# Performance work log

Measured on AMD Instinct MI355X. Metric: run time of the kernel, lower is better.

The kernel has to match this reference:

```python
import jax, jax.numpy as jnp
import numpy as np

B, L, D, H = 2, 2048, 1024, 16
HD = D // H  # head dim = 64


def setup_inputs() -> dict:
    key = jax.random.key(0)
    ks = jax.random.split(key, 5)
    s = 1.0 / np.sqrt(D)
    return {
        "x": jax.random.normal(ks[0], (B, L, D), dtype=jnp.float32),
        "mask": jnp.ones((B, 1, 1, L), dtype=jnp.int32),
        "Wq": jax.random.normal(ks[1], (D, D), dtype=jnp.float32) * s,
        "bq": jnp.zeros((D,), dtype=jnp.float32),
        "Wk": jax.random.normal(ks[2], (D, D), dtype=jnp.float32) * s,
        "bk": jnp.zeros((D,), dtype=jnp.float32),
        "Wv": jax.random.normal(ks[3], (D, D), dtype=jnp.float32) * s,
        "bv": jnp.zeros((D,), dtype=jnp.float32),
        "Wo": jax.random.normal(ks[4], (D, D), dtype=jnp.float32) * s,
        "bo": jnp.zeros((D,), dtype=jnp.float32),
    }


def reference(x, mask, Wq, bq, Wk, bk, Wv, bv, Wo, bo):
    Bx, Lx = x.shape[0], x.shape[1]
    # torch nn.Linear: y = x @ W.T + b
    q = (jnp.einsum("bld,ed->ble", x, Wq) + bq).reshape(Bx, Lx, H, HD).transpose(0, 2, 1, 3)
    k = (jnp.einsum("bld,ed->ble", x, Wk) + bk).reshape(Bx, Lx, H, HD).transpose(0, 2, 1, 3)
    v = (jnp.einsum("bld,ed->ble", x, Wv) + bv).reshape(Bx, Lx, H, HD).transpose(0, 2, 1, 3)
    # [B, H, L, L] scores
    scores = jnp.einsum("bhqd,bhkd->bhqk", q, k) / np.sqrt(HD).astype(np.float32)
    # faithful to original: masked positions are set to the tiny value 1e-9 (not -inf)
    scores = jnp.where(mask == 0, jnp.float32(1e-9), scores)
    attn = jax.nn.softmax(scores, axis=-1)
    # dropout_prob=0.0 -> identity (eval mode)
    out = jnp.einsum("bhqk,bhkd->bhqd", attn, v)  # [B, H, L, HD]
    out = out.transpose(0, 2, 1, 3).reshape(Bx, Lx, D)
    return jnp.einsum("bld,ed->ble", out, Wo) + bo
```

## Files before the change

### kernel.cpp

```cpp
#include <hip/hip_runtime.h>
#include <hip/hip_bf16.h>

typedef _Float16 f16;
typedef _Float16 f16x8 __attribute__((ext_vector_type(8)));
typedef _Float16 f16x4 __attribute__((ext_vector_type(4)));
typedef _Float16 f16x2 __attribute__((ext_vector_type(2)));
typedef float f32x4 __attribute__((ext_vector_type(4)));
typedef int i32x4 __attribute__((ext_vector_type(4)));

#define LDS_LOAD16(gptr, lptr)                                                             \
  __builtin_amdgcn_global_load_lds(                                                        \
      (const __attribute__((address_space(1))) unsigned int*)(gptr),                       \
      (__attribute__((address_space(3))) unsigned int*)(lptr), 16, 0, 0)

#define ALPHA 0.18033688f
#define MASKVAL 1.44269504e-9f

__global__ __launch_bounds__(256) void conv_all(const float* __restrict__ x,
                                                const float* __restrict__ Wq,
                                                const float* __restrict__ Wk,
                                                const float* __restrict__ Wv,
                                                const float* __restrict__ Wo,
                                                f16* __restrict__ xh, f16* __restrict__ wqh,
                                                f16* __restrict__ wkh, f16* __restrict__ wvh,
                                                f16* __restrict__ woh) {
  int i = blockIdx.x * 256 + threadIdx.x;
  const float* src;
  f16* dst;
  int off;
  if (i < 524288) {
    src = x; dst = xh; off = i;
  } else {
    int j = i - 524288;
    int w = j >> 17;
    off = j & 131071;
    src = (w == 0) ? Wq : (w == 1) ? Wk : (w == 2) ? Wv : Wo;
    dst = (w == 0) ? wqh : (w == 1) ? wkh : (w == 2) ? wvh : woh;
  }
  const float4* s4 = (const float4*)src;
  float4 a = s4[2 * off];
  float4 b = s4[2 * off + 1];
  f16x8 o = {(f16)a.x, (f16)a.y, (f16)a.z, (f16)a.w,
             (f16)b.x, (f16)b.y, (f16)b.z, (f16)b.w};
  *(f16x8*)(dst + (size_t)off * 8) = o;
}

__global__ __launch_bounds__(256) void gemm_qkv(const f16* __restrict__ A,
                                                const f16* __restrict__ W0,
                                                const f16* __restrict__ W1,
                                                const f16* __restrict__ W2,
                                                const float* __restrict__ b0,
                                                const float* __restrict__ b1,
                                                const float* __restrict__ b2,
                                                f16* __restrict__ qo, f16* __restrict__ ko,
                                                f16* __restrict__ vo) {
  constexpr int K = 1024, BM = 128, BK = 32;
  __shared__ f16 aT[BM * BK];
  __shared__ f16 bT[BM * BK];
  const int z = blockIdx.z;
  const f16* Bw = (z == 0) ? W0 : (z == 1) ? W1 : W2;
  const float* bias = (z == 0) ? b0 : (z == 1) ? b1 : b2;
  const int tid = threadIdx.x, wid = tid >> 6, lane = tid & 63;
  const int mb = blockIdx.y * BM, nb = blockIdx.x * BM;
  const int wr = wid >> 1, wc = wid & 1;
  const int lr = lane & 15, hi = lane >> 4;

  f32x4 acc[4][4] = {};

  const int r0 = tid >> 2, s0 = tid & 3;
  const int ci1 = 256 + tid, r1 = ci1 >> 2, s1 = ci1 & 3;

  for (int kt = 0; kt < K / BK; ++kt) {
    __syncthreads();
    const int kb = kt * BK;
    LDS_LOAD16(A + (size_t)(mb + r0) * K + kb + s0 * 8, (char*)aT + wid * 1024);
    LDS_LOAD16(Bw + (size_t)(nb + r0) * K + kb + s0 * 8, (char*)bT + wid * 1024);
    LDS_LOAD16(A + (size_t)(mb + r1) * K + kb + s1 * 8, (char*)aT + 4096 + wid * 1024);
    LDS_LOAD16(Bw + (size_t)(nb + r1) * K + kb + s1 * 8, (char*)bT + 4096 + wid * 1024);
    __syncthreads();

    f16x8 af[4], bf[4];
#pragma unroll
    for (int i = 0; i < 4; ++i) af[i] = *(const f16x8*)&aT[(wr * 64 + i * 16 + lr) * BK + hi * 8];
#pragma unroll
    for (int j = 0; j < 4; ++j) bf[j] = *(const f16x8*)&bT[(wc * 64 + j * 16 + lr) * BK + hi * 8];
    __builtin_amdgcn_s_setprio(1);
#pragma unroll
    for (int i = 0; i < 4; ++i)
#pragma unroll
      for (int j = 0; j < 4; ++j)
        acc[i][j] = __builtin_amdgcn_mfma_f32_16x16x32_f16(af[i], bf[j], acc[i][j], 0, 0, 0);
    __builtin_amdgcn_s_setprio(0);
  }

  const float scale = (z == 0) ? ALPHA : 1.0f;
#pragma unroll
  for (int i = 0; i < 4; ++i) {
#pragma unroll
    for (int j = 0; j < 4; ++j) {
      const int row = mb + wr * 64 + i * 16 + hi * 4;
      const int col = nb + wc * 64 + j * 16 + lr;
      const float bv = bias[col];
      const int hh = col >> 6, dd = col & 63;
      if (z == 2) {
        const int bb = row >> 11, l = row & 2047;
        f16x4 v4;
#pragma unroll
        for (int r = 0; r < 4; ++r) v4[r] = (f16)(acc[i][j][r] + bv);
        *(f16x4*)(vo + ((((size_t)bb * 16 + hh) * 64 + dd) * 2048 + l)) = v4;
      } else {
        f16* o = z ? ko : qo;
#pragma unroll
        for (int r = 0; r < 4; ++r) {
          const int m2 = row + r;
          const int bb = m2 >> 11, l = m2 & 2047;
          o[((((size_t)bb * 16 + hh) * 2048 + l) * 64) + dd] = (f16)((acc[i][j][r] + bv) * scale);
        }
      }
    }
  }
}

__global__ __launch_bounds__(256) void gemm_o(const f16* __restrict__ A,
                                              const f16* __restrict__ W,
                                              const float* __restrict__ bias,
                                              float* __restrict__ out) {
  constexpr int K = 1024, N = 1024, BK = 32;
  __shared__ f16 aT[64 * BK];
  __shared__ f16 bT[128 * BK];
  const int tid = threadIdx.x, wid = tid >> 6, lane = tid & 63;
  const int lr = lane & 15, hi = lane >> 4;
  const int mb = blockIdx.y * 64, nb = blockIdx.x * 128;
  const int wr = wid >> 1, wc = wid & 1;
  f32x4 acc[2][4] = {};
  const int ra = tid >> 2, sa = tid & 3;
  const int rb1 = (256 + tid) >> 2, sb1 = (256 + tid) & 3;

  for (int kt = 0; kt < K / BK; ++kt) {
    __syncthreads();
    const int kb = kt * BK;
    LDS_LOAD16(A + (size_t)(mb + ra) * K + kb + sa * 8, (char*)aT + wid * 1024);
    LDS_LOAD16(W + (size_t)(nb + ra) * K + kb + sa * 8, (char*)bT + wid * 1024);
    LDS_LOAD16(W + (size_t)(nb + rb1) * K + kb + sb1 * 8, (char*)bT + 4096 + wid * 1024);
    __syncthreads();
    f16x8 af[2], bf[4];
#pragma unroll
    for (int i = 0; i < 2; ++i) af[i] = *(const f16x8*)&aT[(wr * 32 + i * 16 + lr) * BK + hi * 8];
#pragma unroll
    for (int j = 0; j < 4; ++j) bf[j] = *(const f16x8*)&bT[(wc * 64 + j * 16 + lr) * BK + hi * 8];
    __builtin_amdgcn_s_setprio(1);
#pragma unroll
    for (int i = 0; i < 2; ++i)
#pragma unroll
      for (int j = 0; j < 4; ++j)
        acc[i][j] = __builtin_amdgcn_mfma_f32_16x16x32_f16(af[i], bf[j], acc[i][j], 0, 0, 0);
    __builtin_amdgcn_s_setprio(0);
  }
#pragma unroll
  for (int i = 0; i < 2; ++i)
#pragma unroll
    for (int j = 0; j < 4; ++j) {
      const int col = nb + wc * 64 + j * 16 + lr;
      const float bv = bias[col];
#pragma unroll
      for (int r = 0; r < 4; ++r)
        out[(size_t)(mb + wr * 32 + i * 16 + hi * 4 + r) * N + col] = acc[i][j][r] + bv;
    }
}

__global__ __launch_bounds__(128, 2) void attn2w(const f16* __restrict__ Qh,
                                                 const f16* __restrict__ Kh,
                                                 const f16* __restrict__ Vt,
                                                 const int* __restrict__ mask,
                                                 f16* __restrict__ Oa) {
  constexpr int L = 2048, HD = 64, H = 16, NT = L / 64;
  __shared__ __align__(16) char ldsb[32768];

  const int tid = threadIdx.x, w = tid >> 6, lane = tid & 63;
  const int lr = lane & 15, hi = lane >> 4;
  const int sw = lr & 7;
  const bool oddhi = (hi & 1) != 0;

  const int bid = blockIdx.x;
  const int head = (bid & 7) * 4 + (bid >> 8);
  const int qb = (bid >> 3) & 31;
  const int b = head >> 4, h = head & 15;
  const int qr0 = qb * 64 + w * 32;

  const f16* Qb = Qh + (size_t)head * L * HD;
  const f16* Kb = Kh + (size_t)head * L * HD;
  const f16* Vb = Vt + (size_t)head * HD * L;
  const int* mrow = mask + b * L;

  int mred = 1;
  {
    const int4* m4 = (const int4*)mrow;
#pragma unroll
    for (int j = 0; j < 8; ++j) {
      int4 v = m4[lane + j * 64];
      mred &= v.x & v.y & v.z & v.w;
    }
  }
  const bool allm = __all(mred == 1);

  const int srow = lane >> 3;
  const int schk = (lane & 7) ^ srow;

#define STAGE2W(bb, kt)                                                                     \
  _Pragma("unroll") for (int c = 0; c < 4; ++c) {                                           \
    LDS_LOAD16(Kb + (size_t)((kt) * 64 + w * 32 + c * 8 + srow) * HD + schk * 8,            \
               ldsb + (bb) * 16384 + w * 4096 + c * 1024);                                  \
    LDS_LOAD16(Vb + (size_t)(w * 32 + c * 8 + srow) * L + (kt) * 64 + schk * 8,             \
               ldsb + (bb) * 16384 + 8192 + w * 4096 + c * 1024);                           \
  }

  const char* kbase0 = ldsb + lr * 128 + ((hi ^ sw) * 16);
  const char* kbase1 = ldsb + lr * 128 + (((4 + hi) ^ sw) * 16);

  f16x8 qf[2][2];
#pragma unroll
  for (int qg = 0; qg < 2; ++qg)
#pragma unroll
    for (int k2 = 0; k2 < 2; ++k2)
      qf[qg][k2] = *(const f16x8*)&Qb[(size_t)(qr0 + qg * 16 + lr) * HD + k2 * 32 + hi * 8];

  f32x4 oacc[2][4] = {};
  f32x4 lacc[2] = {};
  const f32x4 zacc = {0.f, 0.f, 0.f, 0.f};
  const f16x8 ones = {1, 1, 1, 1, 1, 1, 1, 1};

  int4 mvA[4], mvB[4];
  if (!allm) {
#pragma unroll
    for (int nf = 0; nf < 4; ++nf) mvA[nf] = *(const int4*)&mrow[nf * 16 + hi * 4];
  }
  STAGE2W(0, 0);

#define ATTN_ITER(kt, P, MVR, MVL)                                                          \
  do {                                                                                      \
    asm volatile("s_waitcnt vmcnt(0)" ::: "memory");                                        \
    __builtin_amdgcn_s_barrier();                                                           \
    if ((kt) + 1 < NT) {                                                                    \
      if (!allm) {                                                                          \
        _Pragma("unroll") for (int nf = 0; nf < 4; ++nf)                                    \
            MVL[nf] = *(const int4*)&mrow[((kt) + 1) * 64 + nf * 16 + hi * 4];              \
      }                                                                                     \
      STAGE2W((P) ^ 1, (kt) + 1);                                                           \
    }                                                                                       \
    f16x8 kf[4][2];                                                                         \
    _Pragma("unroll") for (int nf = 0; nf < 4; ++nf) {                                      \
      kf[nf][0] = *(const f16x8*)(kbase0 + (P) * 16384 + nf * 2048);                        \
      kf[nf][1] = *(const f16x8*)(kbase1 + (P) * 16384 + nf * 2048);                        \
    }                                                                                       \
    f32x4 s[2][4];                                                                          \
    __builtin_amdgcn_s_setprio(1);                                                          \
    _Pragma("unroll") for (int qg = 0; qg < 2; ++qg)                                        \
        _Pragma("unroll") for (int nf = 0; nf < 4; ++nf) {                                  \
      f32x4 z = __builtin_amdgcn_mfma_f32_16x16x32_f16(kf[nf][0], qf[qg][0], zacc, 0, 0, 0);\
      s[qg][nf] = __builtin_amdgcn_mfma_f32_16x16x32_f16(kf[nf][1], qf[qg][1], z, 0, 0, 0); \
    }                                                                                       \
    __builtin_amdgcn_s_setprio(0);                                                          \
    f16x8 pf[2][2];                                                                         \
    _Pragma("unroll") for (int qg = 0; qg < 2; ++qg) {                                      \
      int wpk[4][2];                                                                        \
      _Pragma("unroll") for (int nf = 0; nf < 4; ++nf) {                                    \
        float p0, p1, p2, p3;                                                               \
        if (allm) {                                                                         \
          p0 = __builtin_amdgcn_exp2f(s[qg][nf][0]);                                        \
          p1 = __builtin_amdgcn_exp2f(s[qg][nf][1]);                                        \
          p2 = __builtin_amdgcn_exp2f(s[qg][nf][2]);                                        \
          p3 = __builtin_amdgcn_exp2f(s[qg][nf][3]);                                        \
        } else {                                                                            \
          p0 = __builtin_amdgcn_exp2f(MVR[nf].x ? s[qg][nf][0] : MASKVAL);                  \
          p1 = __builtin_amdgcn_exp2f(MVR[nf].y ? s[qg][nf][1] : MASKVAL);                  \
          p2 = __builtin_amdgcn_exp2f(MVR[nf].z ? s[qg][nf][2] : MASKVAL);                  \
          p3 = __builtin_amdgcn_exp2f(MVR[nf].w ? s[qg][nf][3] : MASKVAL);                  \
        }                                                                                   \
        f16x2 h0 = {(f16)p0, (f16)p1};                                                      \
        f16x2 h1 = {(f16)p2, (f16)p3};                                                      \
        wpk[nf][0] = __builtin_bit_cast(int, h0);                                           \
        wpk[nf][1] = __builtin_bit_cast(int, h1);                                           \
      }                                                                                     \
      _Pragma("unroll") for (int k2 = 0; k2 < 2; ++k2) {                                    \
        int A0 = wpk[2 * k2][0], B0 = wpk[2 * k2 + 1][0];                                   \
        int A1 = wpk[2 * k2][1], B1 = wpk[2 * k2 + 1][1];                                   \
        asm("v_permlane32_swap_b32 %0, %1" : "+v"(A0), "+v"(B0));                           \
        asm("v_permlane32_swap_b32 %0, %1" : "+v"(A1), "+v"(B1));                           \
        int SA0 = __builtin_amdgcn_ds_swizzle(A0, 0x401F);                                  \
        int SB0 = __builtin_amdgcn_ds_swizzle(B0, 0x401F);                                  \
        int SA1 = __builtin_amdgcn_ds_swizzle(A1, 0x401F);                                  \
        int SB1 = __builtin_amdgcn_ds_swizzle(B1, 0x401F);                                  \
        int c0 = oddhi ? SB0 : A0;                                                          \
        int c1 = oddhi ? SB1 : A1;                                                          \
        int c2 = oddhi ? B0 : SA0;                                                          \
        int c3 = oddhi ? B1 : SA1;                                                          \
        i32x4 cc = {c0, c1, c2, c3};                                                        \
        pf[qg][k2] = __builtin_bit_cast(f16x8, cc);                                         \
      }                                                                                     \
    }                                                                                       \
    __builtin_amdgcn_s_setprio(1);                                                          \
    _Pragma("unroll") for (int k2 = 0; k2 < 2; ++k2) {                                      \
      const char* vbase = (k2 ? kbase1 : kbase0) + (P) * 16384 + 8192;                      \
      _Pragma("unroll") for (int df = 0; df < 4; ++df) {                                    \
        f16x8 vf = *(const f16x8*)(vbase + df * 2048);                                      \
        oacc[0][df] = __builtin_amdgcn_mfma_f32_16x16x32_f16(pf[0][k2], vf, oacc[0][df], 0, 0, 0); \
        oacc[1][df] = __builtin_amdgcn_mfma_f32_16x16x32_f16(pf[1][k2], vf, oacc[1][df], 0, 0, 0); \
      }                                                                                     \
      lacc[0] = __builtin_amdgcn_mfma_f32_16x16x32_f16(pf[0][k2], ones, lacc[0], 0, 0, 0);  \
      lacc[1] = __builtin_amdgcn_mfma_f32_16x16x32_f16(pf[1][k2], ones, lacc[1], 0, 0, 0);  \
    }                                                                                       \
    __builtin_amdgcn_s_setprio(0);                                                          \
  } while (0)

  for (int kt = 0; kt < NT; kt += 2) {
    ATTN_ITER(kt, 0, mvA, mvB);
    ATTN_ITER(kt + 1, 1, mvB, mvA);
  }

#pragma unroll
  for (int qg = 0; qg < 2; ++qg) {
    f32x4 rinv;
#pragma unroll
    for (int r = 0; r < 4; ++r) rinv[r] = 1.0f / lacc[qg][r];
#pragma unroll
    for (int df = 0; df < 4; ++df)
#pragma unroll
      for (int r = 0; r < 4; ++r) {
        const int l = qr0 + qg * 16 + hi * 4 + r;
        Oa[(((size_t)b * L + l) * H + h) * HD + df * 16 + lr] = (f16)(oacc[qg][df][r] * rinv[r]);
      }
  }
}

extern "C" void kernel_launch(void* const* d_in, const int* in_sizes, int n_in,
                              void* d_out, int out_size, void* d_ws, size_t ws_size,
                              hipStream_t stream) {
  const float* x  = (const float*)d_in[0];
  const int* mask = (const int*)d_in[1];
  const float* Wq = (const float*)d_in[2];
  const float* bq = (const float*)d_in[3];
  const float* Wk = (const float*)d_in[4];
  const float* bk = (const float*)d_in[5];
  const float* Wv = (const float*)d_in[6];
  const float* bv = (const float*)d_in[7];
  const float* Wo = (const float*)d_in[8];
  const float* bo = (const float*)d_in[9];
  float* out = (float*)d_out;

  char* ws = (char*)d_ws;
  const size_t MB = 1u << 20;
  f16* xh  = (f16*)(ws);
  f16* wqh = (f16*)(ws + 8 * MB);
  f16* wkh = (f16*)(ws + 10 * MB);
  f16* wvh = (f16*)(ws + 12 * MB);
  f16* woh = (f16*)(ws + 14 * MB);
  f16* qh  = (f16*)(ws + 16 * MB);
  f16* kh  = (f16*)(ws + 24 * MB);
  f16* vth = (f16*)(ws + 32 * MB);
  f16* oah = (f16*)(ws + 40 * MB);

  conv_all<<<4096, 256, 0, stream>>>(x, Wq, Wk, Wv, Wo, xh, wqh, wkh, wvh, woh);

  gemm_qkv<<<dim3(8, 32, 3), 256, 0, stream>>>(xh, wqh, wkh, wvh, bq, bk, bv, qh, kh, vth);

  attn2w<<<dim3(1024), 128, 0, stream>>>(qh, kh, vth, mask, oah);

  gemm_o<<<dim3(8, 64), 256, 0, stream>>>(oah, woh, bo, out);
}
```

Measured before the change: 118.7 us.

## Double-buffer LDS tiles in projection GEMMs and use packed f16 conversion in attention

Both projection GEMMs now keep two LDS buffers and issue the global-to-LDS loads for the next K tile before computing on the current one. A partial vmcnt wait lets those loads overlap the MFMA work and replaces the two full syncthreads per iteration. Separately, the attention softmax packs probabilities into f16 pairs with cvt_pkrtz instead of two scalar conversions, which changes rounding to round-toward-zero. The cost is double the LDS footprint in the GEMMs, which could lower occupancy.

```diff
diff --git a/kernel.cpp b/kernel.cpp
--- a/kernel.cpp
+++ b/kernel.cpp
@@ -4,7 +4,6 @@
 typedef _Float16 f16;
 typedef _Float16 f16x8 __attribute__((ext_vector_type(8)));
 typedef _Float16 f16x4 __attribute__((ext_vector_type(4)));
-typedef _Float16 f16x2 __attribute__((ext_vector_type(2)));
 typedef float f32x4 __attribute__((ext_vector_type(4)));
 typedef int i32x4 __attribute__((ext_vector_type(4)));
 
@@ -54,9 +53,9 @@
                                                 const float* __restrict__ b2,
                                                 f16* __restrict__ qo, f16* __restrict__ ko,
                                                 f16* __restrict__ vo) {
-  constexpr int K = 1024, BM = 128, BK = 32;
-  __shared__ f16 aT[BM * BK];
-  __shared__ f16 bT[BM * BK];
+  constexpr int K = 1024, BM = 128, BK = 32, NKT = K / BK;
+  __shared__ f16 aT[2][BM * BK];
+  __shared__ f16 bT[2][BM * BK];
   const int z = blockIdx.z;
   const f16* Bw = (z == 0) ? W0 : (z == 1) ? W1 : W2;
   const float* bias = (z == 0) ? b0 : (z == 1) ? b1 : b2;
@@ -70,20 +69,31 @@
   const int r0 = tid >> 2, s0 = tid & 3;
   const int ci1 = 256 + tid, r1 = ci1 >> 2, s1 = ci1 & 3;
 
-  for (int kt = 0; kt < K / BK; ++kt) {
-    __syncthreads();
-    const int kb = kt * BK;
-    LDS_LOAD16(A + (size_t)(mb + r0) * K + kb + s0 * 8, (char*)aT + wid * 1024);
-    LDS_LOAD16(Bw + (size_t)(nb + r0) * K + kb + s0 * 8, (char*)bT + wid * 1024);
-    LDS_LOAD16(A + (size_t)(mb + r1) * K + kb + s1 * 8, (char*)aT + 4096 + wid * 1024);
-    LDS_LOAD16(Bw + (size_t)(nb + r1) * K + kb + s1 * 8, (char*)bT + 4096 + wid * 1024);
-    __syncthreads();
+#define STAGE_QKV(bb, kt)                                                                   \
+  do {                                                                                      \
+    const int kb_ = (kt) * BK;                                                              \
+    LDS_LOAD16(A + (size_t)(mb + r0) * K + kb_ + s0 * 8, (char*)aT[bb] + wid * 1024);       \
+    LDS_LOAD16(Bw + (size_t)(nb + r0) * K + kb_ + s0 * 8, (char*)bT[bb] + wid * 1024);      \
+    LDS_LOAD16(A + (size_t)(mb + r1) * K + kb_ + s1 * 8, (char*)aT[bb] + 4096 + wid * 1024);\
+    LDS_LOAD16(Bw + (size_t)(nb + r1) * K + kb_ + s1 * 8, (char*)bT[bb] + 4096 + wid * 1024);\
+  } while (0)
+
+  STAGE_QKV(0, 0);
+  for (int kt = 0; kt < NKT; ++kt) {
+    const int p = kt & 1;
+    if (kt + 1 < NKT) {
+      STAGE_QKV(p ^ 1, kt + 1);
+      asm volatile("s_waitcnt vmcnt(4)" ::: "memory");
+    } else {
+      asm volatile("s_waitcnt vmcnt(0)" ::: "memory");
+    }
+    __builtin_amdgcn_s_barrier();
 
     f16x8 af[4], bf[4];
 #pragma unroll
-    for (int i = 0; i < 4; ++i) af[i] = *(const f16x8*)&aT[(wr * 64 + i * 16 + lr) * BK + hi * 8];
-#pragma unroll
-    for (int j = 0; j < 4; ++j) bf[j] = *(const f16x8*)&bT[(wc * 64 + j * 16 + lr) * BK + hi * 8];
+    for (int i = 0; i < 4; ++i) af[i] = *(const f16x8*)&aT[p][(wr * 64 + i * 16 + lr) * BK + hi * 8];
+#pragma unroll
+    for (int j = 0; j < 4; ++j) bf[j] = *(const f16x8*)&bT[p][(wc * 64 + j * 16 + lr) * BK + hi * 8];
     __builtin_amdgcn_s_setprio(1);
 #pragma unroll
     for (int i = 0; i < 4; ++i)
@@ -91,6 +101,7 @@
       for (int j = 0; j < 4; ++j)
         acc[i][j] = __builtin_amdgcn_mfma_f32_16x16x32_f16(af[i], bf[j], acc[i][j], 0, 0, 0);
     __builtin_amdgcn_s_setprio(0);
+    __builtin_amdgcn_s_barrier();
   }
 
   const float scale = (z == 0) ? ALPHA : 1.0f;
@@ -125,9 +136,9 @@
                                               const f16* __restrict__ W,
                                               const float* __restrict__ bias,
                                               float* __restrict__ out) {
-  constexpr int K = 1024, N = 1024, BK = 32;
-  __shared__ f16 aT[64 * BK];
-  __shared__ f16 bT[128 * BK];
+  constexpr int K = 1024, N = 1024, BK = 32, NKT = K / BK;
+  __shared__ f16 aT[2][64 * BK];
+  __shared__ f16 bT[2][128 * BK];
   const int tid = threadIdx.x, wid = tid >> 6, lane = tid & 63;
   const int lr = lane & 15, hi = lane >> 4;
   const int mb = blockIdx.y * 64, nb = blockIdx.x * 128;
@@ -136,18 +147,29 @@
   const int ra = tid >> 2, sa = tid & 3;
   const int rb1 = (256 + tid) >> 2, sb1 = (256 + tid) & 3;
 
-  for (int kt = 0; kt < K / BK; ++kt) {
-    __syncthreads();
-    const int kb = kt * BK;
-    LDS_LOAD16(A + (size_t)(mb + ra) * K + kb + sa * 8, (char*)aT + wid * 1024);
-    LDS_LOAD16(W + (size_t)(nb + ra) * K + kb + sa * 8, (char*)bT + wid * 1024);
-    LDS_LOAD16(W + (size_t)(nb + rb1) * K + kb + sb1 * 8, (char*)bT + 4096 + wid * 1024);
-    __syncthreads();
+#define STAGE_O(bb, kt)                                                                     \
+  do {                                                                                      \
+    const int kb_ = (kt) * BK;                                                              \
+    LDS_LOAD16(A + (size_t)(mb + ra) * K + kb_ + sa * 8, (char*)aT[bb] + wid * 1024);       \
+    LDS_LOAD16(W + (size_t)(nb + ra) * K + kb_ + sa * 8, (char*)bT[bb] + wid * 1024);       \
+    LDS_LOAD16(W + (size_t)(nb + rb1) * K + kb_ + sb1 * 8, (char*)bT[bb] + 4096 + wid * 1024);\
+  } while (0)
+
+  STAGE_O(0, 0);
+  for (int kt = 0; kt < NKT; ++kt) {
+    const int p = kt & 1;
+    if (kt + 1 < NKT) {
+      STAGE_O(p ^ 1, kt + 1);
+      asm volatile("s_waitcnt vmcnt(3)" ::: "memory");
+    } else {
+      asm volatile("s_waitcnt vmcnt(0)" ::: "memory");
+    }
+    __builtin_amdgcn_s_barrier();
     f16x8 af[2], bf[4];
 #pragma unroll
-    for (int i = 0; i < 2; ++i) af[i] = *(const f16x8*)&aT[(wr * 32 + i * 16 + lr) * BK + hi * 8];
-#pragma unroll
-    for (int j = 0; j < 4; ++j) bf[j] = *(const f16x8*)&bT[(wc * 64 + j * 16 + lr) * BK + hi * 8];
+    for (int i = 0; i < 2; ++i) af[i] = *(const f16x8*)&aT[p][(wr * 32 + i * 16 + lr) * BK + hi * 8];
+#pragma unroll
+    for (int j = 0; j < 4; ++j) bf[j] = *(const f16x8*)&bT[p][(wc * 64 + j * 16 + lr) * BK + hi * 8];
     __builtin_amdgcn_s_setprio(1);
 #pragma unroll
     for (int i = 0; i < 2; ++i)
@@ -155,6 +177,7 @@
       for (int j = 0; j < 4; ++j)
         acc[i][j] = __builtin_amdgcn_mfma_f32_16x16x32_f16(af[i], bf[j], acc[i][j], 0, 0, 0);
     __builtin_amdgcn_s_setprio(0);
+    __builtin_amdgcn_s_barrier();
   }
 #pragma unroll
   for (int i = 0; i < 2; ++i)
@@ -276,10 +299,8 @@
           p2 = __builtin_amdgcn_exp2f(MVR[nf].z ? s[qg][nf][2] : MASKVAL);                  \
           p3 = __builtin_amdgcn_exp2f(MVR[nf].w ? s[qg][nf][3] : MASKVAL);                  \
         }                                                                                   \
-        f16x2 h0 = {(f16)p0, (f16)p1};                                                      \
-        f16x2 h1 = {(f16)p2, (f16)p3};                                                      \
-        wpk[nf][0] = __builtin_bit_cast(int, h0);                                           \
-        wpk[nf][1] = __builtin_bit_cast(int, h1);                                           \
+        wpk[nf][0] = __builtin_bit_cast(int, __builtin_amdgcn_cvt_pkrtz(p0, p1));           \
+        wpk[nf][1] = __builtin_bit_cast(int, __builtin_amdgcn_cvt_pkrtz(p2, p3));           \
       }                                                                                     \
       _Pragma("unroll") for (int k2 = 0; k2 < 2; ++k2) {                                    \
         int A0 = wpk[2 * k2][0], B0 = wpk[2 * k2 + 1][0];                                   \
```

After: 119.7 us. No clear change (+0.9%).
